# Optimization experiments

Hardware: AMD Instinct MI355X
Metric: run time of the kernel (lower is better)

## Reference

```python
import jax, jax.numpy as jnp
import numpy as np

# ---- config (YOLOv4-style, TRAIN_SIZE=608, P2..P5) ----
STRIDES = (4.0, 8.0, 16.0, 32.0)
ANCHORS = np.array([
    [[12, 16], [19, 36], [40, 28], [36, 75]],
    [[36, 75], [76, 55], [72, 146], [142, 110]],
    [[72, 146], [142, 110], [192, 243], [459, 401]],
    [[142, 110], [192, 243], [300, 300], [459, 401]],
], dtype=np.float32)  # [LEVELS, NUM_ANCHORS, 2]
MAX_PROP = 100
SCORE_THRESH = 0.25
IOU_THRESH = 0.5


def decode_prediction(p, anchors, stride):
    # p: [b, A, h, w, 6] -> [b, A*h*w, 5] with xyxy + score
    b, A, h, w, _ = p.shape
    txy, twh, conf, cls = p[..., :2], p[..., 2:4], p[..., 4:5], p[..., 5:6]
    gx, gy = jnp.meshgrid(jnp.arange(w, dtype=p.dtype), jnp.arange(h, dtype=p.dtype))
    grid = jnp.stack([gx, gy], axis=-1)[None, None]  # [1,1,h,w,2]
    xy = (jax.nn.sigmoid(txy) + grid) * stride
    wh = jnp.exp(twh) * anchors[None, :, None, None, :]
    score = jax.nn.sigmoid(conf) * jax.nn.sigmoid(cls)
    x1y1 = xy - 0.5 * wh
    x2y2 = xy + 0.5 * wh
    out = jnp.concatenate([x1y1, x2y2, score], axis=-1)  # [b,A,h,w,5]
    return out.reshape(b, A * h * w, 5)


def _iou_one_vs_all(box, boxes):
    # box: [4], boxes: [N,4] (xyxy)
    lt = jnp.maximum(box[:2], boxes[:, :2])
    rb = jnp.minimum(box[2:], boxes[:, 2:])
    wh = jnp.maximum(rb - lt, 0.0)
    inter = wh[:, 0] * wh[:, 1]
    a1 = jnp.maximum(box[2] - box[0], 0.0) * jnp.maximum(box[3] - box[1], 0.0)
    a2 = jnp.maximum(boxes[:, 2] - boxes[:, 0], 0.0) * jnp.maximum(boxes[:, 3] - boxes[:, 1], 0.0)
    return inter / (a1 + a2 - inter + 1e-9)


def _nms_single(boxes, scores):
    # greedy NMS, padded to MAX_PROP with zero rows
    s0 = jnp.where(scores >= SCORE_THRESH, scores, 0.0)

    def step(s, _):
        i = jnp.argmax(s)
        sc = s[i]
        box = boxes[i]
        keep = sc > 0.0
        row = jnp.where(keep, jnp.concatenate([box, sc[None]]), jnp.zeros(5, boxes.dtype))
        iou = _iou_one_vs_all(box, boxes)
        s = jnp.where((iou > IOU_THRESH) & keep, 0.0, s)
        s = s.at[i].set(0.0)
        return s, row

    _, props = jax.lax.scan(step, s0, None, length=MAX_PROP)
    return props  # [MAX_PROP, 5]


def entry_stop_gradients(t, mask):
    # gradient flows only through entries where mask==1
    return jax.lax.stop_gradient(t) * (1.0 - mask) + t * mask


def _forward(p2, p3, p4, p5):
    anchors = jnp.asarray(ANCHORS)
    d2 = decode_prediction(p2, anchors[0], STRIDES[0])
    d3 = decode_prediction(p3, anchors[1], STRIDES[1])
    d4 = decode_prediction(p4, anchors[2], STRIDES[2])
    d5 = decode_prediction(p5, anchors[3], STRIDES[3])
    proposals = jnp.concatenate([d2, d3, d4, d5], axis=1)  # [b, N, 5]
    proposals = jax.vmap(lambda pr: _nms_single(pr[:, :4], pr[:, 4]))(proposals)  # [b, MAX_PROP, 5]
    mask = (jnp.sum(proposals[..., :4], axis=-1) != 0.0).astype(proposals.dtype)[..., None]
    return entry_stop_gradients(proposals, mask)


def setup_inputs() -> dict:
    key = jax.random.key(0)
    k2, k3, k4, k5 = jax.random.split(key, 4)
    b, A, ch = 32, 4, 6
    return {
        "p2": jax.random.normal(k2, (b, A, 152, 152, ch), dtype=jnp.float32),
        "p3": jax.random.normal(k3, (b, A, 76, 76, ch), dtype=jnp.float32),
        "p4": jax.random.normal(k4, (b, A, 38, 38, ch), dtype=jnp.float32),
        "p5": jax.random.normal(k5, (b, A, 19, 19, ch), dtype=jnp.float32),
    }


def reference(p2, p3, p4, p5):
    return _forward(p2, p3, p4, p5)
```

## Files before the change

kernel.cpp:

```cpp
#include <hip/hip_runtime.h>
#include <cstdint>
#include <cstddef>

typedef unsigned int u32;
typedef unsigned long long u64;

#define NTOT 122740
#define NPAIR 61370
#define KTOP 1024
#define WIN  256
#define NBIN 4096
#define SCORE_T 0.25f
#define TBITS 0x3E800000u

#define RT0 0x3F5DF000u
#define RT1 0x3F3FF000u
#define RT2 0x3F1FF000u
#define RT3 0x3EFFF000u

#define CSTRIDE 128
#define CAP0 4096
#define CAP1 8192
#define CAP2 12288
#define CAP3 16384
#define CAP4 16384
#define OFF0 0
#define OFF1 4096
#define OFF2 12288
#define OFF3 24576
#define OFF4 40960
#define BATCH_ENT 57344

#define F4TOT 184110
#define F4B3 138624
#define F4B4 173280
#define F4B5 181944

#define WS_CAND 16384

__device__ __forceinline__ float sigm(float x) { return 1.0f / (1.0f + expf(-x)); }

__device__ __forceinline__ int score_bin(u32 bits) {
  return min(4095, 1 + (int)((bits - TBITS) >> 12));
}

__device__ __forceinline__ u64 shfl_u64(u64 x, int src) {
  int lo = __shfl((int)(u32)x, src, 64);
  int hi = __shfl((int)(u32)(x >> 32), src, 64);
  return ((u64)(u32)hi << 32) | (u32)lo;
}

__device__ __forceinline__ void score_pair(int P, int b,
    const float* __restrict__ p2, const float* __restrict__ p3,
    const float* __restrict__ p4, const float* __restrict__ p5,
    u32& b0, u32& b1, u32& gi0, u32& gi1)
{
  int t0 = 2 * P;
  const float* p; int l0, LN;
  if (t0 < 92416)       { p = p2; l0 = t0;          LN = 92416; }
  else if (t0 < 115520) { p = p3; l0 = t0 - 92416;  LN = 23104; }
  else if (t0 < 121296) { p = p4; l0 = t0 - 115520; LN = 5776;  }
  else                  { p = p5; l0 = t0 - 121296; LN = 1444;  }
  const float* q = p + ((size_t)b * LN + (size_t)l0) * 6;
  float4 v1 = *(const float4*)(q + 4);
  float4 v2 = *(const float4*)(q + 8);
  float s0 = sigm(v1.x) * sigm(v1.y);
  float s1 = sigm(v2.z) * sigm(v2.w);
  b0 = (s0 >= SCORE_T) ? __float_as_uint(s0) : 0u;
  b1 = (s1 >= SCORE_T) ? __float_as_uint(s1) : 0u;
  gi0 = (u32)t0; gi1 = (u32)(t0 + 1);
}

__device__ float4 decode_box_from_gidx(u32 gidx, int b,
    const float* __restrict__ p2, const float* __restrict__ p3,
    const float* __restrict__ p4, const float* __restrict__ p5)
{
  const float* p; int t, H, W; float stride;
  float aw0, ah0, aw1, ah1, aw2, ah2, aw3, ah3;
  if (gidx < 92416u) {
    p = p2 + (size_t)b * 92416 * 6; t = (int)gidx; H = 152; W = 152; stride = 4.0f;
    aw0=12.f; ah0=16.f; aw1=19.f; ah1=36.f; aw2=40.f; ah2=28.f; aw3=36.f; ah3=75.f;
  } else if (gidx < 115520u) {
    p = p3 + (size_t)b * 23104 * 6; t = (int)(gidx - 92416u); H = 76; W = 76; stride = 8.0f;
    aw0=36.f; ah0=75.f; aw1=76.f; ah1=55.f; aw2=72.f; ah2=146.f; aw3=142.f; ah3=110.f;
  } else if (gidx < 121296u) {
    p = p4 + (size_t)b * 5776 * 6; t = (int)(gidx - 115520u); H = 38; W = 38; stride = 16.0f;
    aw0=72.f; ah0=146.f; aw1=142.f; ah1=110.f; aw2=192.f; ah2=243.f; aw3=459.f; ah3=401.f;
  } else {
    p = p5 + (size_t)b * 1444 * 6; t = (int)(gidx - 121296u); H = 19; W = 19; stride = 32.0f;
    aw0=142.f; ah0=110.f; aw1=192.f; ah1=243.f; aw2=300.f; ah2=300.f; aw3=459.f; ah3=401.f;
  }
  int HW = H * W;
  int a = t / HW;
  int r = t - a * HW;
  int y = r / W;
  int x = r - y * W;
  const float* q = p + (size_t)t * 6;
  float2 t01 = *(const float2*)(q + 0);
  float2 t23 = *(const float2*)(q + 2);
  float cx = (sigm(t01.x) + (float)x) * stride;
  float cy = (sigm(t01.y) + (float)y) * stride;
  float aw = (a == 0) ? aw0 : (a == 1) ? aw1 : (a == 2) ? aw2 : aw3;
  float ah = (a == 0) ? ah0 : (a == 1) ? ah1 : (a == 2) ? ah2 : ah3;
  float bw = expf(t23.x) * aw;
  float bh = expf(t23.y) * ah;
  return make_float4(cx - 0.5f * bw, cy - 0.5f * bh, cx + 0.5f * bw, cy + 0.5f * bh);
}

__device__ __forceinline__ bool iou_gt(float4 A, float4 B) {
  float ltx = fmaxf(A.x, B.x), lty = fmaxf(A.y, B.y);
  float rbx = fminf(A.z, B.z), rby = fminf(A.w, B.w);
  float w = fmaxf(rbx - ltx, 0.0f), h = fmaxf(rby - lty, 0.0f);
  float inter = w * h;
  float a1 = fmaxf(A.z - A.x, 0.0f) * fmaxf(A.w - A.y, 0.0f);
  float a2 = fmaxf(B.z - B.x, 0.0f) * fmaxf(B.w - B.y, 0.0f);
  float iou = inter / (a1 + a2 - inter + 1e-9f);
  return iou > 0.5f;
}

__global__ __launch_bounds__(512)
void decode_kernel(const float* __restrict__ p2, const float* __restrict__ p3,
                   const float* __restrict__ p4, const float* __restrict__ p5,
                   u32* __restrict__ counters, uint2* __restrict__ cand)
{
  __shared__ float4 sbuf4[1536];
  __shared__ uint2 stg[1024];
  __shared__ u32 lcnt[8], lseg[8], lrank[8], gbase[8];
  const int tid = threadIdx.x;
  const int b = blockIdx.y;
  if (tid < 8) { lcnt[tid] = 0u; lrank[tid] = 0u; gbase[tid] = 0u; }

  const int rbase = blockIdx.x * 1024;
  const int FS = blockIdx.x * 1536;
  const float4* q2 = (const float4*)p2;
  const float4* q3 = (const float4*)p3;
  const float4* q4 = (const float4*)p4;
  const float4* q5 = (const float4*)p5;
  #pragma unroll
  for (int j = 0; j < 3; ++j) {
    int idx4 = FS + j * 512 + tid;
    if (idx4 < F4TOT) {
      const float4* src;
      if (idx4 < F4B3)      src = q2 + (size_t)b * 138624 + idx4;
      else if (idx4 < F4B4) src = q3 + (size_t)b * 34656  + (idx4 - F4B3);
      else if (idx4 < F4B5) src = q4 + (size_t)b * 8664   + (idx4 - F4B4);
      else                  src = q5 + (size_t)b * 2166   + (idx4 - F4B5);
      sbuf4[j * 512 + tid] = *src;
    }
  }
  __syncthreads();

  const float* sbuf = (const float*)sbuf4;
  u32 kb[2]; u32 kg[2]; int kr[2];
  #pragma unroll
  for (int k = 0; k < 2; ++k) {
    kb[k] = 0u; kr[k] = -1;
    int lr = tid + k * 512;
    int rg = rbase + lr;
    kg[k] = (u32)rg;
    if (rg < NTOT) {
      float2 cc = *(const float2*)&sbuf[lr * 6 + 4];
      float s = sigm(cc.x) * sigm(cc.y);
      if (s >= SCORE_T) {
        u32 bb = __float_as_uint(s);
        kb[k] = bb;
        int r;
        if      (bb >= RT0) r = 0;
        else if (bb >= RT1) r = 1;
        else if (bb >= RT2) r = 2;
        else if (bb >= RT3) r = 3;
        else                r = 4;
        kr[k] = r;
        atomicAdd(&lcnt[r], 1u);
      }
    }
  }
  __syncthreads();
  if (tid == 0) {
    u32 s = 0;
    #pragma unroll
    for (int r = 0; r < 5; ++r) { lseg[r] = s; s += lcnt[r]; }
  }
  if (tid < 5 && lcnt[tid]) gbase[tid] = atomicAdd(&counters[(size_t)b * CSTRIDE + tid * 16], lcnt[tid]);
  __syncthreads();
  #pragma unroll
  for (int k = 0; k < 2; ++k) {
    if (kr[k] >= 0) {
      u32 rk = atomicAdd(&lrank[kr[k]], 1u);
      stg[lseg[kr[k]] + rk] = make_uint2(kb[k], kg[k]);
    }
  }
  __syncthreads();
  uint2* cb = cand + (size_t)b * BATCH_ENT;
  const u32 roff[5] = { OFF0, OFF1, OFF2, OFF3, OFF4 };
  const u32 rcap[5] = { CAP0, CAP1, CAP2, CAP3, CAP4 };
  #pragma unroll
  for (int r = 0; r < 5; ++r) {
    const u32 cnt = lcnt[r], sg = lseg[r], gb = gbase[r];
    for (u32 i = tid; i < cnt; i += 512) {
      u32 d = gb + i;
      if (d < rcap[r]) cb[roff[r] + d] = stg[sg + i];
    }
  }
}

__global__ __launch_bounds__(1024, 1)
void mega_kernel(const u32* __restrict__ counters, const uint2* __restrict__ cand,
                 const float* __restrict__ p2, const float* __restrict__ p3,
                 const float* __restrict__ p4, const float* __restrict__ p5,
                 float* __restrict__ out)
{
  const int b = blockIdx.x;
  const int tid = threadIdx.x;

  __shared__ u32 sstart[NBIN];
  __shared__ u32 scur[NBIN];
  __shared__ u64 skey[KTOP];
  __shared__ u64 skey2[KTOP];
  __shared__ float4 sbox[WIN];
  __shared__ u64 smat[WIN * 4];
  __shared__ float4 selbox[100];
  __shared__ int s_misc[4];
  __shared__ int s_B, s_n;

  const u32 c0 = counters[(size_t)b * CSTRIDE +  0];
  const u32 c1 = counters[(size_t)b * CSTRIDE + 16];
  const u32 c2 = counters[(size_t)b * CSTRIDE + 32];
  const u32 c3 = counters[(size_t)b * CSTRIDE + 48];
  const u32 c4 = counters[(size_t)b * CSTRIDE + 64];
  const u32 total = c0 + c1 + c2 + c3 + c4;
  const u32 need = min((u32)KTOP, total);
  int RL = 0;
  { u32 cum = c0;
    if (cum < need) { RL = 1; cum += c1; }
    if (cum < need) { RL = 2; cum += c2; }
    if (cum < need) { RL = 3; cum += c3; }
    if (cum < need) { RL = 4; cum += c4; }
  }
  const bool fb = (c0 > (u32)CAP0)
               || (RL >= 1 && c1 > (u32)CAP1)
               || (RL >= 2 && c2 > (u32)CAP2)
               || (RL >= 3 && c3 > (u32)CAP3)
               || (RL >= 4 && c4 > (u32)CAP4);

  for (int i = tid; i < NBIN; i += 1024) scur[i] = 0u;
  __syncthreads();

  const uint2* cb = cand + (size_t)b * BATCH_ENT;

  if (!fb) {
    for (u32 i = tid; i < c0; i += 1024) atomicAdd(&scur[score_bin(cb[OFF0 + i].x)], 1u);
    if (RL >= 1) for (u32 i = tid; i < c1; i += 1024) atomicAdd(&scur[score_bin(cb[OFF1 + i].x)], 1u);
    if (RL >= 2) for (u32 i = tid; i < c2; i += 1024) atomicAdd(&scur[score_bin(cb[OFF2 + i].x)], 1u);
    if (RL >= 3) for (u32 i = tid; i < c3; i += 1024) atomicAdd(&scur[score_bin(cb[OFF3 + i].x)], 1u);
    if (RL >= 4) for (u32 i = tid; i < c4; i += 1024) atomicAdd(&scur[score_bin(cb[OFF4 + i].x)], 1u);
  } else {
    for (int P = tid; P < NPAIR; P += 1024) {
      u32 b0, b1, gi0, gi1;
      score_pair(P, b, p2, p3, p4, p5, b0, b1, gi0, gi1);
      if (b0) atomicAdd(&scur[score_bin(b0)], 1u);
      if (b1) atomicAdd(&scur[score_bin(b1)], 1u);
    }
  }
  __syncthreads();

  if (tid < 64) {
    u32 h[64];
    #pragma unroll
    for (int k = 0; k < 64; ++k) h[k] = scur[tid * 64 + k];
    u32 lsum = 0;
    #pragma unroll
    for (int k = 0; k < 64; ++k) lsum += h[k];
    u32 S = lsum;
    #pragma unroll
    for (int off = 1; off < 64; off <<= 1) {
      u32 v = (u32)__shfl_down((int)S, off, 64);
      if (tid + off < 64) S += v;
    }
    u32 c = S - lsum;
    int Bv = -1; u32 nv = 0;
    for (int k = 63; k >= 0; --k) {
      sstart[tid * 64 + k] = c;
      c += h[k];
      if (c <= (u32)KTOP) { Bv = tid * 64 + k; nv = c; }
    }
    u32 pk = (Bv < 0) ? 0xFFFFFFFFu : (((u32)Bv << 12) | nv);
    #pragma unroll
    for (int off = 32; off >= 1; off >>= 1) {
      u32 o = (u32)__shfl_down((int)pk, off, 64);
      if (tid + off < 64) pk = min(pk, o);
    }
    if (tid == 0) {
      if (pk == 0xFFFFFFFFu) { s_B = 4095; s_n = KTOP; }
      else { s_B = max((int)(pk >> 12), 1); s_n = (int)(pk & 0xFFFu); }
    }
  }
  __syncthreads();
  const int B = s_B;
  const int n = min(s_n, KTOP);

  for (int i = tid; i < NBIN; i += 1024) scur[i] = sstart[i];
  __syncthreads();

  if (!fb) {
    for (u32 i = tid; i < c0; i += 1024) {
      uint2 e = cb[OFF0 + i]; int bin = score_bin(e.x);
      if (bin >= B) { u32 sl = atomicAdd(&scur[bin], 1u);
        if (sl < (u32)KTOP) skey[sl] = ((u64)e.x << 32) | (u32)(~e.y); }
    }
    if (RL >= 1) for (u32 i = tid; i < c1; i += 1024) {
      uint2 e = cb[OFF1 + i]; int bin = score_bin(e.x);
      if (bin >= B) { u32 sl = atomicAdd(&scur[bin], 1u);
        if (sl < (u32)KTOP) skey[sl] = ((u64)e.x << 32) | (u32)(~e.y); }
    }
    if (RL >= 2) for (u32 i = tid; i < c2; i += 1024) {
      uint2 e = cb[OFF2 + i]; int bin = score_bin(e.x);
      if (bin >= B) { u32 sl = atomicAdd(&scur[bin], 1u);
        if (sl < (u32)KTOP) skey[sl] = ((u64)e.x << 32) | (u32)(~e.y); }
    }
    if (RL >= 3) for (u32 i = tid; i < c3; i += 1024) {
      uint2 e = cb[OFF3 + i]; int bin = score_bin(e.x);
      if (bin >= B) { u32 sl = atomicAdd(&scur[bin], 1u);
        if (sl < (u32)KTOP) skey[sl] = ((u64)e.x << 32) | (u32)(~e.y); }
    }
    if (RL >= 4) for (u32 i = tid; i < c4; i += 1024) {
      uint2 e = cb[OFF4 + i]; int bin = score_bin(e.x);
      if (bin >= B) { u32 sl = atomicAdd(&scur[bin], 1u);
        if (sl < (u32)KTOP) skey[sl] = ((u64)e.x << 32) | (u32)(~e.y); }
    }
  } else {
    for (int P = tid; P < NPAIR; P += 1024) {
      u32 b0, b1, gi0, gi1;
      score_pair(P, b, p2, p3, p4, p5, b0, b1, gi0, gi1);
      if (b0) { int bin = score_bin(b0);
        if (bin >= B) { u32 sl = atomicAdd(&scur[bin], 1u);
          if (sl < (u32)KTOP) skey[sl] = ((u64)b0 << 32) | (u32)(~gi0); } }
      if (b1) { int bin = score_bin(b1);
        if (bin >= B) { u32 sl = atomicAdd(&scur[bin], 1u);
          if (sl < (u32)KTOP) skey[sl] = ((u64)b1 << 32) | (u32)(~gi1); } }
    }
  }
  __syncthreads();

  for (int s = tid; s < n; s += 1024) {
    u64 k = skey[s];
    int bin = score_bin((u32)(k >> 32));
    int st = (int)sstart[bin];
    int en = (int)scur[bin];
    u32 r = 0;
    for (int j = st; j < en; ++j) r += (skey[j] > k) ? 1u : 0u;
    skey2[st + r] = k;
  }
  __syncthreads();

  const int Wn = min(n, WIN);

  if (tid < WIN) {
    sbox[tid] = (tid < Wn) ? decode_box_from_gidx(~(u32)skey2[tid], b, p2, p3, p4, p5)
                           : make_float4(0.f, 0.f, 0.f, 0.f);
  }
  __syncthreads();

  {
    int row = tid & 255, word = tid >> 8;
    u64 bits = 0;
    if (row < Wn) {
      float4 A = sbox[row];
      int j0 = word * 64;
      int je = min(64, Wn - j0);
      for (int j = 0; j < je; ++j)
        if (iou_gt(A, sbox[j0 + j])) bits |= (1ull << j);
    }
    smat[word * 256 + row] = bits;
  }
  __syncthreads();

  if (tid < 64) {
    const int lane = tid;
    u64 m0[4], m1[4], m2[4], m3[4];
    #pragma unroll
    for (int w = 0; w < 4; ++w) {
      m0[w] = smat[w * 256 +   0 + lane];
      m1[w] = smat[w * 256 +  64 + lane];
      m2[w] = smat[w * 256 + 128 + lane];
      m3[w] = smat[w * 256 + 192 + lane];
    }
    u64 live[4];
    #pragma unroll
    for (int g2 = 0; g2 < 4; ++g2) {
      int lo = g2 * 64;
      live[g2] = (Wn >= lo + 64) ? ~0ull : (Wn > lo ? ((1ull << (Wn - lo)) - 1ull) : 0ull);
    }
    int sel = 0;
    #pragma unroll 1
    for (int w2 = 0; w2 < 4; ++w2) {
      while (live[w2] && sel < 100) {
        int j = (int)__ffsll(live[w2]) - 1;
        int p = (w2 << 6) + j;
        u64 r0, r1, r2, r3;
        if (w2 == 0)      { r0 = shfl_u64(m0[0], j); r1 = shfl_u64(m0[1], j); r2 = shfl_u64(m0[2], j); r3 = shfl_u64(m0[3], j); }
        else if (w2 == 1) { r0 = shfl_u64(m1[0], j); r1 = shfl_u64(m1[1], j); r2 = shfl_u64(m1[2], j); r3 = shfl_u64(m1[3], j); }
        else if (w2 == 2) { r0 = shfl_u64(m2[0], j); r1 = shfl_u64(m2[1], j); r2 = shfl_u64(m2[2], j); r3 = shfl_u64(m2[3], j); }
        else              { r0 = shfl_u64(m3[0], j); r1 = shfl_u64(m3[1], j); r2 = shfl_u64(m3[2], j); r3 = shfl_u64(m3[3], j); }
        live[0] &= ~r0; live[1] &= ~r1; live[2] &= ~r2; live[3] &= ~r3;
        live[w2] &= ~(1ull << j);
        if (lane == 0) {
          float4 box = sbox[p];
          u64 k = skey2[p];
          float sc = __uint_as_float((u32)(k >> 32));
          selbox[sel] = box;
          float* orow = out + (size_t)b * 500 + (size_t)sel * 5;
          orow[0] = box.x; orow[1] = box.y; orow[2] = box.z; orow[3] = box.w; orow[4] = sc;
        }
        sel++;
      }
    }
    if (lane == 0) {
      s_misc[2] = sel;
      s_misc[3] = (sel < 100 && n > WIN) ? 1 : 0;
    }
  }
  __syncthreads();

  if (s_misc[3]) {
    if (tid < 64) {
      const int lane = tid;
      int sel = s_misc[2];
      for (int p = WIN; p < n && sel < 100; ++p) {
        u64 k = skey2[p];
        float4 box = decode_box_from_gidx(~(u32)k, b, p2, p3, p4, p5);
        bool hit = false;
        if (lane < sel) hit = iou_gt(selbox[lane], box);
        if (lane + 64 < sel) hit = hit || iou_gt(selbox[lane + 64], box);
        u64 anyhit = __ballot(hit);
        if (anyhit == 0ull) {
          if (lane == 0) {
            selbox[sel] = box;
            float sc = __uint_as_float((u32)(k >> 32));
            float* orow = out + (size_t)b * 500 + (size_t)sel * 5;
            orow[0] = box.x; orow[1] = box.y; orow[2] = box.z; orow[3] = box.w; orow[4] = sc;
          }
          sel++;
        }
      }
      if (lane == 0) s_misc[2] = sel;
    }
  }
  __syncthreads();

  const int nsel = s_misc[2];
  for (int i = tid; i < (100 - nsel) * 5; i += 1024)
    out[(size_t)b * 500 + (size_t)nsel * 5 + i] = 0.0f;
}

extern "C" void kernel_launch(void* const* d_in, const int* in_sizes, int n_in,
                              void* d_out, int out_size, void* d_ws, size_t ws_size,
                              hipStream_t stream) {
  const float* p2 = (const float*)d_in[0];
  const float* p3 = (const float*)d_in[1];
  const float* p4 = (const float*)d_in[2];
  const float* p5 = (const float*)d_in[3];
  float* out = (float*)d_out;

  unsigned char* w = (unsigned char*)d_ws;
  u32*   counters = (u32*)w;
  uint2* cand     = (uint2*)(w + WS_CAND);

  hipMemsetAsync(counters, 0, 32 * CSTRIDE * sizeof(u32), stream);
  decode_kernel<<<dim3(120, 32), 512, 0, stream>>>(p2, p3, p4, p5, counters, cand);
  mega_kernel<<<32, 1024, 0, stream>>>(counters, cand, p2, p3, p4, p5, out);
}
```

Baseline: 176.2 us.

## Score directly from float4 loads, halve decode grid, parallelize histogram scan

The decode kernel no longer stages inputs in shared memory. Each thread now reads six float4 values and scores the conf/cls pairs that sit in the second and third float4 of each 6-float record, so each block covers twice as many records and the grid is halved. In the mega kernel, the 4096-bin histogram prefix scan and the top-K bin search are spread over all 16 waves with a cross-wave reduction, replacing a single-wave loop over 64 bins per lane. The trade is extra registers and redundant float4 loads, one third of which carry only box coordinates and are discarded, in exchange for removing the LDS staging and a serial scan.

```diff
diff --git a/kernel.cpp b/kernel.cpp
--- a/kernel.cpp
+++ b/kernel.cpp
@@ -35,6 +35,8 @@
 #define F4B3 138624
 #define F4B4 173280
 #define F4B5 181944
+
+#define F4_PER_BLK 3072
 
 #define WS_CAND 16384
 
@@ -123,55 +125,49 @@
                    const float* __restrict__ p4, const float* __restrict__ p5,
                    u32* __restrict__ counters, uint2* __restrict__ cand)
 {
-  __shared__ float4 sbuf4[1536];
-  __shared__ uint2 stg[1024];
+  __shared__ uint2 stg[2048];
   __shared__ u32 lcnt[8], lseg[8], lrank[8], gbase[8];
   const int tid = threadIdx.x;
   const int b = blockIdx.y;
   if (tid < 8) { lcnt[tid] = 0u; lrank[tid] = 0u; gbase[tid] = 0u; }
-
-  const int rbase = blockIdx.x * 1024;
-  const int FS = blockIdx.x * 1536;
+  __syncthreads();
+
   const float4* q2 = (const float4*)p2;
   const float4* q3 = (const float4*)p3;
   const float4* q4 = (const float4*)p4;
   const float4* q5 = (const float4*)p5;
+  const int FS = blockIdx.x * F4_PER_BLK;
+
+  u32 kb[6]; u32 kg6[6]; int kr6[6];
   #pragma unroll
-  for (int j = 0; j < 3; ++j) {
-    int idx4 = FS + j * 512 + tid;
-    if (idx4 < F4TOT) {
+  for (int k = 0; k < 6; ++k) {
+    kb[k] = 0u; kr6[k] = -1; kg6[k] = 0u;
+    int i4 = FS + k * 512 + tid;
+    if (i4 < F4TOT) {
       const float4* src;
-      if (idx4 < F4B3)      src = q2 + (size_t)b * 138624 + idx4;
-      else if (idx4 < F4B4) src = q3 + (size_t)b * 34656  + (idx4 - F4B3);
-      else if (idx4 < F4B5) src = q4 + (size_t)b * 8664   + (idx4 - F4B4);
-      else                  src = q5 + (size_t)b * 2166   + (idx4 - F4B5);
-      sbuf4[j * 512 + tid] = *src;
-    }
-  }
-  __syncthreads();
-
-  const float* sbuf = (const float*)sbuf4;
-  u32 kb[2]; u32 kg[2]; int kr[2];
-  #pragma unroll
-  for (int k = 0; k < 2; ++k) {
-    kb[k] = 0u; kr[k] = -1;
-    int lr = tid + k * 512;
-    int rg = rbase + lr;
-    kg[k] = (u32)rg;
-    if (rg < NTOT) {
-      float2 cc = *(const float2*)&sbuf[lr * 6 + 4];
-      float s = sigm(cc.x) * sigm(cc.y);
-      if (s >= SCORE_T) {
-        u32 bb = __float_as_uint(s);
-        kb[k] = bb;
-        int r;
-        if      (bb >= RT0) r = 0;
-        else if (bb >= RT1) r = 1;
-        else if (bb >= RT2) r = 2;
-        else if (bb >= RT3) r = 3;
-        else                r = 4;
-        kr[k] = r;
-        atomicAdd(&lcnt[r], 1u);
+      if (i4 < F4B3)      src = q2 + (size_t)b * 138624 + i4;
+      else if (i4 < F4B4) src = q3 + (size_t)b * 34656  + (i4 - F4B3);
+      else if (i4 < F4B5) src = q4 + (size_t)b * 8664   + (i4 - F4B4);
+      else                src = q5 + (size_t)b * 2166   + (i4 - F4B5);
+      float4 v = *src;
+      int k3 = i4 / 3;
+      int trib = i4 - 3 * k3;
+      if (trib) {
+        float cf = (trib == 1) ? v.x : v.z;
+        float cl = (trib == 1) ? v.y : v.w;
+        float s = sigm(cf) * sigm(cl);
+        if (s >= SCORE_T) {
+          u32 bb = __float_as_uint(s);
+          int r;
+          if      (bb >= RT0) r = 0;
+          else if (bb >= RT1) r = 1;
+          else if (bb >= RT2) r = 2;
+          else if (bb >= RT3) r = 3;
+          else                r = 4;
+          kb[k] = bb; kr6[k] = r;
+          kg6[k] = (u32)(2 * k3 + (trib - 1));
+          atomicAdd(&lcnt[r], 1u);
+        }
       }
     }
   }
@@ -184,10 +180,10 @@
   if (tid < 5 && lcnt[tid]) gbase[tid] = atomicAdd(&counters[(size_t)b * CSTRIDE + tid * 16], lcnt[tid]);
   __syncthreads();
   #pragma unroll
-  for (int k = 0; k < 2; ++k) {
-    if (kr[k] >= 0) {
-      u32 rk = atomicAdd(&lrank[kr[k]], 1u);
-      stg[lseg[kr[k]] + rk] = make_uint2(kb[k], kg[k]);
+  for (int k = 0; k < 6; ++k) {
+    if (kr6[k] >= 0) {
+      u32 rk = atomicAdd(&lrank[kr6[k]], 1u);
+      stg[lseg[kr6[k]] + rk] = make_uint2(kb[k], kg6[k]);
     }
   }
   __syncthreads();
@@ -212,9 +208,11 @@
 {
   const int b = blockIdx.x;
   const int tid = threadIdx.x;
-
-  __shared__ u32 sstart[NBIN];
-  __shared__ u32 scur[NBIN];
+  const int lane = tid & 63, wv = tid >> 6;
+
+  __shared__ __align__(16) u32 sstart[NBIN];
+  __shared__ __align__(16) u32 scur[NBIN];
+  __shared__ u32 wred[16];
   __shared__ u64 skey[KTOP];
   __shared__ u64 skey2[KTOP];
   __shared__ float4 sbox[WIN];
@@ -243,7 +241,7 @@
                || (RL >= 3 && c3 > (u32)CAP3)
                || (RL >= 4 && c4 > (u32)CAP4);
 
-  for (int i = tid; i < NBIN; i += 1024) scur[i] = 0u;
+  ((uint4*)scur)[tid] = make_uint4(0u, 0u, 0u, 0u);
   __syncthreads();
 
   const uint2* cb = cand + (size_t)b * BATCH_ENT;
@@ -264,42 +262,53 @@
   }
   __syncthreads();
 
-  if (tid < 64) {
-    u32 h[64];
-    #pragma unroll
-    for (int k = 0; k < 64; ++k) h[k] = scur[tid * 64 + k];
-    u32 lsum = 0;
-    #pragma unroll
-    for (int k = 0; k < 64; ++k) lsum += h[k];
+  {
+    uint4 hv = ((const uint4*)scur)[tid];
+    u32 loc4[4] = { hv.x, hv.y, hv.z, hv.w };
+    u32 lsum = hv.x + hv.y + hv.z + hv.w;
     u32 S = lsum;
     #pragma unroll
     for (int off = 1; off < 64; off <<= 1) {
       u32 v = (u32)__shfl_down((int)S, off, 64);
-      if (tid + off < 64) S += v;
-    }
-    u32 c = S - lsum;
-    int Bv = -1; u32 nv = 0;
-    for (int k = 63; k >= 0; --k) {
-      sstart[tid * 64 + k] = c;
-      c += h[k];
-      if (c <= (u32)KTOP) { Bv = tid * 64 + k; nv = c; }
-    }
-    u32 pk = (Bv < 0) ? 0xFFFFFFFFu : (((u32)Bv << 12) | nv);
+      if (lane + off < 64) S += v;
+    }
+    u32 wtot = (u32)__shfl((int)S, 0, 64);
+    if (lane == 0) wred[wv] = wtot;
+    __syncthreads();
+    u32 U = 0;
+    for (int w2 = wv + 1; w2 < 16; ++w2) U += wred[w2];
+    u32 T = U + (S - lsum);
+    u32 ss[4];
+    u32 run = T;
+    #pragma unroll
+    for (int j = 3; j >= 0; --j) { ss[j] = run; run += loc4[j]; }
+    ((uint4*)sstart)[tid] = make_uint4(ss[0], ss[1], ss[2], ss[3]);
+    u32 pk = 0xFFFFFFFFu;
+    #pragma unroll
+    for (int j = 0; j < 4; ++j) {
+      u32 cge = ss[j] + loc4[j];
+      if (pk == 0xFFFFFFFFu && cge <= (u32)KTOP) pk = ((u32)(4 * tid + j) << 12) | cge;
+    }
     #pragma unroll
     for (int off = 32; off >= 1; off >>= 1) {
       u32 o = (u32)__shfl_down((int)pk, off, 64);
-      if (tid + off < 64) pk = min(pk, o);
-    }
+      if (lane + off < 64) pk = min(pk, o);
+    }
+    __syncthreads();
+    if (lane == 0) wred[wv] = pk;
+    __syncthreads();
     if (tid == 0) {
-      if (pk == 0xFFFFFFFFu) { s_B = 4095; s_n = KTOP; }
-      else { s_B = max((int)(pk >> 12), 1); s_n = (int)(pk & 0xFFFu); }
+      u32 m = 0xFFFFFFFFu;
+      for (int w2 = 0; w2 < 16; ++w2) m = min(m, wred[w2]);
+      if (m == 0xFFFFFFFFu) { s_B = 4095; s_n = KTOP; }
+      else { s_B = max((int)(m >> 12), 1); s_n = (int)(m & 0xFFFu); }
     }
   }
   __syncthreads();
   const int B = s_B;
   const int n = min(s_n, KTOP);
 
-  for (int i = tid; i < NBIN; i += 1024) scur[i] = sstart[i];
+  ((uint4*)scur)[tid] = ((const uint4*)sstart)[tid];
   __syncthreads();
 
   if (!fb) {
@@ -376,7 +385,6 @@
   __syncthreads();
 
   if (tid < 64) {
-    const int lane = tid;
     u64 m0[4], m1[4], m2[4], m3[4];
     #pragma unroll
     for (int w = 0; w < 4; ++w) {
@@ -424,7 +432,6 @@
 
   if (s_misc[3]) {
     if (tid < 64) {
-      const int lane = tid;
       int sel = s_misc[2];
       for (int p = WIN; p < n && sel < 100; ++p) {
         u64 k = skey2[p];
@@ -467,6 +474,6 @@
   uint2* cand     = (uint2*)(w + WS_CAND);
 
   hipMemsetAsync(counters, 0, 32 * CSTRIDE * sizeof(u32), stream);
-  decode_kernel<<<dim3(120, 32), 512, 0, stream>>>(p2, p3, p4, p5, counters, cand);
+  decode_kernel<<<dim3(60, 32), 512, 0, stream>>>(p2, p3, p4, p5, counters, cand);
   mega_kernel<<<32, 1024, 0, stream>>>(counters, cand, p2, p3, p4, p5, out);
 }
```

Result: no change. 173.5 us (-1.5%).
